# Kernel tuning notes

Hardware: AMD Instinct MI355X
Metric: run time of the kernel (lower is better)

Reference implementation:

```python
import jax, jax.numpy as jnp
import numpy as np
import itertools

D_FEAT = 8      # feature dim per point
N_NBR = 16     # kNN neighbors (self.N)
ORDERS = (2, 3)
BIG = 99999999.0


def _to_select(N, order):
    # rows: [0] + each (order-1)-combination of {1..N-1}, first N-1 rows
    rows = [[0] + list(c) for c in itertools.combinations(range(1, N), order - 1)][:N - 1]
    return np.asarray(rows, dtype=np.int32)  # (N-1, order)


def setup_inputs() -> dict:
    key = jax.random.key(0)
    ks = jax.random.split(key, 18)
    B, NP, DM, DO, NM, PNM = 4, 4096, 16, 8, 64, 64
    r = lambda k, s: jax.random.normal(k, s, dtype=jnp.float32)
    return {
        "x": r(ks[0], (B, NP * D_FEAT)),
        "z": r(ks[1], (B, PNM)),
        "Wm2": r(ks[2], (2, DM)) * 0.5, "bm2": r(ks[3], (DM,)) * 0.1,
        "Wm3": r(ks[4], (3, DM)) * 0.5, "bm3": r(ks[5], (DM,)) * 0.1,
        "Wv2": r(ks[6], (2, DM)) * 0.5, "bv2": r(ks[7], (DM,)) * 0.1,
        "Wv3": r(ks[8], (3, DM)) * 0.5, "bv3": r(ks[9], (DM,)) * 0.1,
        "Wmx": r(ks[10], (2 * DM, DO)) * 0.1, "bmx": r(ks[11], (DO,)) * 0.1,
        "Wvx": r(ks[12], (2 * DM, NM)) * 0.1, "bvx": r(ks[13], (NM,)) * 0.1,
        "Wmz": r(ks[14], (PNM, DO)) * 0.1, "bmz": r(ks[15], (DO,)) * 0.1,
        "Wvz": r(ks[16], (PNM, NM)) * 0.1, "bvz": r(ks[17], (NM,)) * 0.1,
    }


def _forward(x, z, Wm2, bm2, Wm3, bm3, Wv2, bv2, Wv3, bv3,
             Wmx, bmx, Wvx, bvx, Wmz, bmz, Wvz, bvz):
    B = x.shape[0]
    NP = x.shape[1] // D_FEAT
    N = N_NBR
    x3 = x.reshape(B, NP, D_FEAT)

    # pairwise euclidean distances via gram trick (avoids B*NP*NP*D intermediate)
    n2 = jnp.sum(x3 * x3, axis=-1)                                   # (B, NP)
    d2 = n2[:, :, None] + n2[:, None, :] - 2.0 * jnp.einsum('bid,bjd->bij', x3, x3)
    dist = jnp.sqrt(jnp.maximum(d2, 0.0))                            # (B, NP, NP)
    dist = jnp.where(dist == 0.0, BIG, dist)                         # mask exact-zero distances
    diag = jnp.arange(NP)
    dist = dist.at[:, diag, diag].set(BIG)                           # self-distance (exactly 0 in torch)

    # N smallest, sorted ascending
    _, idx = jax.lax.top_k(-dist, N)                                 # idx: (B, NP, N)

    def order_feats(Wf, bf, order):
        ts = jnp.asarray(_to_select(N, order))                       # (N-1, order)
        sel = idx[:, :, ts]                                          # (B, NP, N-1, o)
        g = jax.vmap(lambda xb, sb: xb[sb])(x3, sel)                 # (B, NP, N-1, o, D)
        # Linear(order -> d_Mfeat) applied per feature-dim o-tuple, relu, mean over feature dims
        y = jax.nn.relu(jnp.einsum('bnrod,ok->bnrdk', g, Wf) + bf)   # (B, NP, N-1, D, K)
        return y.mean(axis=3).reshape(B, NP * (N - 1), -1)           # (B, NP*(N-1), K)

    moments = jnp.concatenate([order_feats(Wm2, bm2, 2), order_feats(Wm3, bm3, 3)], axis=-1)
    v_moments = jnp.concatenate([order_feats(Wv2, bv2, 2), order_feats(Wv3, bv3, 3)], axis=-1)

    d_out = Wmx.shape[1]
    x_new = jax.nn.relu(moments @ Wmx + bmx + (z @ Wmz + bmz)[:, None, :])
    x_new = x_new.reshape(B, NP, N - 1, d_out).mean(axis=2).reshape(B, NP * d_out)

    z_new = jax.nn.relu(v_moments @ Wvx + bvx + (z @ Wvz + bvz)[:, None, :]).mean(axis=1)
    return x_new, z_new


def reference(x, z, Wm2, bm2, Wm3, bm3, Wv2, bv2, Wv3, bv3,
              Wmx, bmx, Wvx, bvx, Wmz, bmz, Wvz, bvz):
    return _forward(x, z, Wm2, bm2, Wm3, bm3, Wv2, bv2, Wv3, bv3,
                    Wmx, bmx, Wvx, bvx, Wmz, bmz, Wvz, bvz)
```

## Files before the change

kernel.cpp:

```cpp
#include <hip/hip_runtime.h>
#include <hip/hip_bf16.h>

#define BIGF 99999999.0f
#define NPP 4096
#define BB 4
#define NQ 4


__device__ __forceinline__ float rl(float v, int l) {
    return __int_as_float(__builtin_amdgcn_readlane(__float_as_int(v), l));
}

template <typename T>
__device__ __forceinline__ T bitonic_sort64(T v, int lane) {
    #pragma unroll
    for (int k = 2; k <= 64; k <<= 1) {
        #pragma unroll
        for (int j = k >> 1; j > 0; j >>= 1) {
            T p = __shfl_xor(v, j);
            bool up  = ((lane & k) == 0);
            bool low = ((lane & j) == 0);
            T mn = (v < p) ? v : p;
            T mx = (v < p) ? p : v;
            v = (up == low) ? mn : mx;
        }
    }
    return v;
}

__device__ __forceinline__ unsigned d2key(const float* qf, float n2i,
                                          const float4& a, const float4& c,
                                          float n2j, int j, int q) {
    float dot = 0.f;
    dot = fmaf(qf[0], a.x, dot); dot = fmaf(qf[1], a.y, dot);
    dot = fmaf(qf[2], a.z, dot); dot = fmaf(qf[3], a.w, dot);
    dot = fmaf(qf[4], c.x, dot); dot = fmaf(qf[5], c.y, dot);
    dot = fmaf(qf[6], c.z, dot); dot = fmaf(qf[7], c.w, dot);
    float d2 = fmaf(-2.0f, dot, n2i + n2j);
    return (d2 <= 0.0f || j == q) ? __float_as_uint(BIGF) : __float_as_uint(d2);
}


__global__ __launch_bounds__(256) void n2_kernel(const float* __restrict__ x,
                                                 float* __restrict__ n2tab,
                                                 float* __restrict__ zout) {
    int i = blockIdx.x * 256 + threadIdx.x;
    if (blockIdx.x == 0) zout[threadIdx.x] = 0.f;
    const float4* p = (const float4*)(x + (long)i * 8);
    float4 a = p[0], c = p[1];
    float s = 0.f;
    s = fmaf(a.x, a.x, s); s = fmaf(a.y, a.y, s);
    s = fmaf(a.z, a.z, s); s = fmaf(a.w, a.w, s);
    s = fmaf(c.x, c.x, s); s = fmaf(c.y, c.y, s);
    s = fmaf(c.z, c.z, s); s = fmaf(c.w, c.w, s);
    n2tab[i] = s;
}


__global__ void zz_kernel(const float* __restrict__ z,
                          const float* __restrict__ Wmz, const float* __restrict__ bmz,
                          const float* __restrict__ Wvz, const float* __restrict__ bvz,
                          float* __restrict__ zzm, float* __restrict__ zzv) {
    int b = blockIdx.x, l = threadIdx.x;
    float sv = 0.f;
    for (int p = 0; p < 64; ++p) sv = fmaf(z[b * 64 + p], Wvz[p * 64 + l], sv);
    zzv[b * 64 + l] = sv + bvz[l];
    if (l < 8) {
        float sm = 0.f;
        for (int p = 0; p < 64; ++p) sm = fmaf(z[b * 64 + p], Wmz[p * 8 + l], sm);
        zzm[b * 8 + l] = sm + bmz[l];
    }
}


__global__ __launch_bounds__(256) void knn_kernel(const float* __restrict__ x,
                                                  const float* __restrict__ n2tab,
                                                  int* __restrict__ idx_out) {
    __shared__ unsigned long long cand[4][NQ][64];

    int lane = threadIdx.x & 63;
    int wid  = threadIdx.x >> 6;
    int gw   = blockIdx.x * 4 + wid;
    int q0   = gw * NQ;
    int b    = q0 >> 12;
    int qloc = q0 & 4095;
    const float* xb = x + (long)b * NPP * 8;
    const float* nb = n2tab + b * NPP;

    float qf[NQ][8];
    float n2i[NQ];
    #pragma unroll
    for (int q = 0; q < NQ; ++q) {
        #pragma unroll
        for (int f = 0; f < 8; ++f) qf[q][f] = xb[(qloc + q) * 8 + f];
        n2i[q] = nb[qloc + q];
    }

    unsigned minb[NQ];
    #pragma unroll
    for (int q = 0; q < NQ; ++q) minb[q] = 0xFFFFFFFFu;

    #pragma unroll 4
    for (int t = 0; t < 64; ++t) {
        int j = t * 64 + lane;
        const float4* pj = (const float4*)(xb + j * 8);
        float4 a = pj[0], c = pj[1];
        float n2j = nb[j];
        #pragma unroll
        for (int q = 0; q < NQ; ++q) {
            unsigned kb = d2key(qf[q], n2i[q], a, c, n2j, j, qloc + q);
            minb[q] = (kb < minb[q]) ? kb : minb[q];
        }
    }

    unsigned T[NQ];
    #pragma unroll
    for (int q = 0; q < NQ; ++q) {
        unsigned v = bitonic_sort64(minb[q], lane);
        T[q] = (unsigned)__shfl((int)v, 15);
    }

    int cnt[NQ];
    #pragma unroll
    for (int q = 0; q < NQ; ++q) cnt[q] = 0;

    for (int t = 0; t < 64; ++t) {
        int j = t * 64 + lane;
        const float4* pj = (const float4*)(xb + j * 8);
        float4 a = pj[0], c = pj[1];
        float n2j = nb[j];
        #pragma unroll
        for (int q = 0; q < NQ; ++q) {
            unsigned kb = d2key(qf[q], n2i[q], a, c, n2j, j, qloc + q);
            bool pred = (kb <= T[q]);
            unsigned long long m = __ballot(pred);
            if (m) {
                int ofs = cnt[q] + __popcll(m & ((1ull << lane) - 1ull));
                if (pred && ofs < 64) {
                    cand[wid][q][ofs] = ((unsigned long long)kb << 32) | (unsigned)j;
                }
                cnt[q] += __popcll(m);
            }
        }
    }

    #pragma unroll 1
    for (int q = 0; q < NQ; ++q) {
        int c = cnt[q] < 64 ? cnt[q] : 64;
        unsigned long long key = (lane < c) ? cand[wid][q][lane] : ~0ull;
        key = bitonic_sort64(key, lane);
        if (lane < 16) {
            idx_out[(long)(q0 + q) * 16 + lane] = (int)(key & 0xFFFFFFFFull);
        }
    }
}


__global__ __launch_bounds__(256) void feat_kernel(
    const float* __restrict__ x, const int* __restrict__ idxw,
    const float* __restrict__ Wm2, const float* __restrict__ bm2,
    const float* __restrict__ Wm3, const float* __restrict__ bm3,
    const float* __restrict__ Wv2, const float* __restrict__ bv2,
    const float* __restrict__ Wv3, const float* __restrict__ bv3,
    const float* __restrict__ Wmx, const float* __restrict__ bmx,
    const float* __restrict__ Wvx, const float* __restrict__ bvx,
    const float* __restrict__ zzm, const float* __restrict__ zzv,
    float* __restrict__ xout, float* __restrict__ zout)
{
    int lane = threadIdx.x & 63;
    int wid  = threadIdx.x >> 6;
    int pn   = blockIdx.x * 4 + wid;
    int b    = pn >> 12;
    const float* xb = x + b * NPP * 8;

    __shared__ float xg_s[4][16][8];
    __shared__ float mm_s[4][15][36];
    __shared__ float wmx_s[32][8];
    __shared__ float bzm_s[8];
    __shared__ float zpart[4][64];

    if (threadIdx.x < 256) {
        wmx_s[threadIdx.x >> 3][threadIdx.x & 7] = Wmx[threadIdx.x];
    }
    if (threadIdx.x < 8) bzm_s[threadIdx.x] = bmx[threadIdx.x] + zzm[b * 8 + threadIdx.x];

    int k = lane & 15;
    float w20 = Wm2[k], w21 = Wm2[16 + k], bb2 = bm2[k];
    float w30 = Wm3[k], w31 = Wm3[16 + k], w32 = Wm3[32 + k], bb3 = bm3[k];
    float u20 = Wv2[k], u21 = Wv2[16 + k], cc2 = bv2[k];
    float u30 = Wv3[k], u31 = Wv3[16 + k], u32 = Wv3[32 + k], cc3 = bv3[k];
    float wvx[32];
    #pragma unroll
    for (int c = 0; c < 32; ++c) wvx[c] = Wvx[c * 64 + lane];
    float bz3 = bvx[lane] + zzv[b * 64 + lane];

    if (lane < 16) {
        int myid = idxw[(long)pn * 16 + lane];
        const float4* ps = (const float4*)(xb + (long)myid * 8);
        float4 a = ps[0], c4 = ps[1];
        *((float4*)&xg_s[wid][lane][0]) = a;
        *((float4*)&xg_s[wid][lane][4]) = c4;
    }
    __syncthreads();

    float g0[8];
    #pragma unroll
    for (int f = 0; f < 8; ++f) g0[f] = xg_s[wid][0][f];

    float am2[4], am3[4], av2[4], av3[4];
    #pragma unroll
    for (int p = 0; p < 4; ++p) {
        int rg = lane >> 4;
        int r  = p * 4 + rg;
        int rc = (r < 14) ? r : 14;
        int i2  = rc + 1;
        int i3a = (rc < 14) ? 1 : 2;
        int i3b = (rc < 14) ? rc + 2 : 3;
        const float* G1  = xg_s[wid][i2];
        const float* G3a = xg_s[wid][i3a];
        const float* G3b = xg_s[wid][i3b];
        float s2 = 0.f, s3 = 0.f, t2 = 0.f, t3 = 0.f;
        #pragma unroll
        for (int d = 0; d < 8; ++d) {
            float gz = g0[d], g1 = G1[d], ga = G3a[d], gb = G3b[d];
            float y2 = fmaf(gz, w20, fmaf(g1, w21, bb2));
            s2 += fmaxf(y2, 0.f);
            float y3 = fmaf(gz, w30, fmaf(ga, w31, fmaf(gb, w32, bb3)));
            s3 += fmaxf(y3, 0.f);
            float z2 = fmaf(gz, u20, fmaf(g1, u21, cc2));
            t2 += fmaxf(z2, 0.f);
            float z3 = fmaf(gz, u30, fmaf(ga, u31, fmaf(gb, u32, cc3)));
            t3 += fmaxf(z3, 0.f);
        }
        am2[p] = s2 * 0.125f; am3[p] = s3 * 0.125f;
        av2[p] = t2 * 0.125f; av3[p] = t3 * 0.125f;
        if (r < 15) {
            mm_s[wid][r][k]      = am2[p];
            mm_s[wid][r][16 + k] = am3[p];
        }
    }
    __syncthreads();

    float xa = 0.f;
    #pragma unroll
    for (int half = 0; half < 2; ++half) {
        int r   = (lane >> 3) + half * 8;
        int doo = lane & 7;
        float s = 0.f;
        if (r < 15) {
            s = bzm_s[doo];
            #pragma unroll
            for (int c = 0; c < 32; ++c)
                s = fmaf(mm_s[wid][r][c], wmx_s[c][doo], s);
            s = fmaxf(s, 0.f);
        }
        xa += s;
    }
    xa += __shfl_xor(xa, 8);
    xa += __shfl_xor(xa, 16);
    xa += __shfl_xor(xa, 32);
    float xv = xa * (1.0f / 15.0f);
    if (lane < 8) xout[(long)pn * 8 + lane] = xv;

    float za = 0.f;
    #pragma unroll
    for (int r = 0; r < 15; ++r) {
        float s = bz3;
        const int p  = r >> 2;
        const int sb = (r & 3) * 16;
        #pragma unroll
        for (int c = 0; c < 16; ++c)
            s = fmaf(rl(av2[p], sb + c), wvx[c], s);
        #pragma unroll
        for (int c = 0; c < 16; ++c)
            s = fmaf(rl(av3[p], sb + c), wvx[16 + c], s);
        za += fmaxf(s, 0.f);
    }
    za *= (1.0f / 61440.0f);

    zpart[wid][lane] = za;
    __syncthreads();
    if (wid == 0) {
        float ssum = zpart[0][lane] + zpart[1][lane] + zpart[2][lane] + zpart[3][lane];
        atomicAdd(&zout[b * 64 + lane], ssum);
    }
}


extern "C" void kernel_launch(void* const* d_in, const int* in_sizes, int n_in,
                              void* d_out, int out_size, void* d_ws, size_t ws_size,
                              hipStream_t stream) {
    const float* x   = (const float*)d_in[0];
    const float* z   = (const float*)d_in[1];
    const float* Wm2 = (const float*)d_in[2];
    const float* bm2 = (const float*)d_in[3];
    const float* Wm3 = (const float*)d_in[4];
    const float* bm3 = (const float*)d_in[5];
    const float* Wv2 = (const float*)d_in[6];
    const float* bv2 = (const float*)d_in[7];
    const float* Wv3 = (const float*)d_in[8];
    const float* bv3 = (const float*)d_in[9];
    const float* Wmx = (const float*)d_in[10];
    const float* bmx = (const float*)d_in[11];
    const float* Wvx = (const float*)d_in[12];
    const float* bvx = (const float*)d_in[13];
    const float* Wmz = (const float*)d_in[14];
    const float* bmz = (const float*)d_in[15];
    const float* Wvz = (const float*)d_in[16];
    const float* bvz = (const float*)d_in[17];

    float* out  = (float*)d_out;
    int*   idxw = (int*)d_ws;
    float* zzm  = (float*)((char*)d_ws + (size_t)BB * NPP * 16 * 4);
    float* zzv  = zzm + BB * 8;
    float* n2t  = zzv + BB * 64;
    float* xout = out;
    float* zout = out + BB * NPP * 8;

    n2_kernel<<<dim3(BB * NPP / 256), dim3(256), 0, stream>>>(x, n2t, zout);
    zz_kernel<<<dim3(BB), dim3(64), 0, stream>>>(z, Wmz, bmz, Wvz, bvz, zzm, zzv);
    knn_kernel<<<dim3(BB * NPP / (4 * NQ)), dim3(256), 0, stream>>>(x, n2t, idxw);
    feat_kernel<<<dim3(4096), dim3(256), 0, stream>>>(
        x, idxw, Wm2, bm2, Wm3, bm3, Wv2, bv2, Wv3, bv3,
        Wmx, bmx, Wvx, bvx, zzm, zzv, xout, zout);
}
```

Before: 266.7 us.

## Precompute kNN thresholds in separate kernel and merge larger candidate sets

Moves the threshold pass out of knn_kernel into a new thr_kernel. In it, each lane handles one query and takes minima over 16 strided stripes, and the maximum of those 16 minima serves as an upper bound for the 16th-nearest distance. knn_kernel then does only the ballot-compaction pass, with a larger candidate buffer (256 per query) and a chunked bitonic merge. The self-index check becomes cheaper and the zero-distance masking is dropped. The looser threshold lets more candidates through, which adds merge work and shared-memory use in exchange for removing one full distance pass per wavefront.

```diff
diff --git a/kernel.cpp b/kernel.cpp
--- a/kernel.cpp
+++ b/kernel.cpp
@@ -5,6 +5,7 @@
 #define NPP 4096
 #define BB 4
 #define NQ 4
+#define CAP 256
 
 
 __device__ __forceinline__ float rl(float v, int l) {
@@ -26,18 +27,6 @@
         }
     }
     return v;
-}
-
-__device__ __forceinline__ unsigned d2key(const float* qf, float n2i,
-                                          const float4& a, const float4& c,
-                                          float n2j, int j, int q) {
-    float dot = 0.f;
-    dot = fmaf(qf[0], a.x, dot); dot = fmaf(qf[1], a.y, dot);
-    dot = fmaf(qf[2], a.z, dot); dot = fmaf(qf[3], a.w, dot);
-    dot = fmaf(qf[4], c.x, dot); dot = fmaf(qf[5], c.y, dot);
-    dot = fmaf(qf[6], c.z, dot); dot = fmaf(qf[7], c.w, dot);
-    float d2 = fmaf(-2.0f, dot, n2i + n2j);
-    return (d2 <= 0.0f || j == q) ? __float_as_uint(BIGF) : __float_as_uint(d2);
 }
 
 
@@ -73,10 +62,65 @@
 }
 
 
+__global__ __launch_bounds__(512) void thr_kernel(const float* __restrict__ x,
+                                                  const float* __restrict__ n2tab,
+                                                  unsigned* __restrict__ Ttab) {
+    __shared__ unsigned mins_s[16][64];
+
+    int lane = threadIdx.x & 63;
+    int wid  = threadIdx.x >> 6;
+    int qg   = blockIdx.x * 64 + lane;
+    int b    = qg >> 12;
+    int qloc = qg & 4095;
+    const float* xb = x + (long)b * NPP * 8;
+    const float* nb = n2tab + b * NPP;
+
+    float qf[8];
+    #pragma unroll
+    for (int f = 0; f < 8; ++f) qf[f] = xb[(long)qloc * 8 + f];
+    float n2i = nb[qloc];
+    const unsigned BIGB = __float_as_uint(BIGF);
+
+    unsigned m0 = 0xFFFFFFFFu, m1 = 0xFFFFFFFFu;
+    int j0 = wid * 512;
+    #pragma unroll 4
+    for (int i = 0; i < 512; ++i) {
+        int j = j0 + i;
+        const float4* pj = (const float4*)(xb + (long)j * 8);
+        float4 a = pj[0], c = pj[1];
+        float n2j = nb[j];
+        float dot = 0.f;
+        dot = fmaf(qf[0], a.x, dot); dot = fmaf(qf[1], a.y, dot);
+        dot = fmaf(qf[2], a.z, dot); dot = fmaf(qf[3], a.w, dot);
+        dot = fmaf(qf[4], c.x, dot); dot = fmaf(qf[5], c.y, dot);
+        dot = fmaf(qf[6], c.z, dot); dot = fmaf(qf[7], c.w, dot);
+        float d2 = fmaf(-2.0f, dot, n2i + n2j);
+        unsigned kb = __float_as_uint(d2);
+        kb = (j == qloc) ? BIGB : kb;
+        if (i & 1) { m1 = (kb < m1) ? kb : m1; }
+        else       { m0 = (kb < m0) ? kb : m0; }
+    }
+    mins_s[wid * 2 + 0][lane] = m0;
+    mins_s[wid * 2 + 1][lane] = m1;
+    __syncthreads();
+
+    if (wid == 0) {
+        unsigned T = 0;
+        #pragma unroll
+        for (int i = 0; i < 16; ++i) {
+            unsigned v = mins_s[i][lane];
+            T = (v > T) ? v : T;
+        }
+        Ttab[blockIdx.x * 64 + lane] = T;
+    }
+}
+
+
 __global__ __launch_bounds__(256) void knn_kernel(const float* __restrict__ x,
                                                   const float* __restrict__ n2tab,
+                                                  const unsigned* __restrict__ Ttab,
                                                   int* __restrict__ idx_out) {
-    __shared__ unsigned long long cand[4][NQ][64];
+    __shared__ unsigned long long cand[4][NQ][CAP];
 
     int lane = threadIdx.x & 63;
     int wid  = threadIdx.x >> 6;
@@ -89,54 +133,45 @@
 
     float qf[NQ][8];
     float n2i[NQ];
+    unsigned Tq[NQ];
+    int cnt[NQ], selfT[NQ], selfL[NQ];
     #pragma unroll
     for (int q = 0; q < NQ; ++q) {
         #pragma unroll
         for (int f = 0; f < 8; ++f) qf[q][f] = xb[(qloc + q) * 8 + f];
-        n2i[q] = nb[qloc + q];
-    }
-
-    unsigned minb[NQ];
-    #pragma unroll
-    for (int q = 0; q < NQ; ++q) minb[q] = 0xFFFFFFFFu;
-
-    #pragma unroll 4
+        n2i[q]   = nb[qloc + q];
+        Tq[q]    = Ttab[q0 + q];
+        cnt[q]   = 0;
+        selfT[q] = (qloc + q) >> 6;
+        selfL[q] = (qloc + q) & 63;
+    }
+    const unsigned BIGB = __float_as_uint(BIGF);
+
     for (int t = 0; t < 64; ++t) {
         int j = t * 64 + lane;
-        const float4* pj = (const float4*)(xb + j * 8);
+        const float4* pj = (const float4*)(xb + (long)j * 8);
         float4 a = pj[0], c = pj[1];
         float n2j = nb[j];
         #pragma unroll
         for (int q = 0; q < NQ; ++q) {
-            unsigned kb = d2key(qf[q], n2i[q], a, c, n2j, j, qloc + q);
-            minb[q] = (kb < minb[q]) ? kb : minb[q];
-        }
-    }
-
-    unsigned T[NQ];
-    #pragma unroll
-    for (int q = 0; q < NQ; ++q) {
-        unsigned v = bitonic_sort64(minb[q], lane);
-        T[q] = (unsigned)__shfl((int)v, 15);
-    }
-
-    int cnt[NQ];
-    #pragma unroll
-    for (int q = 0; q < NQ; ++q) cnt[q] = 0;
-
-    for (int t = 0; t < 64; ++t) {
-        int j = t * 64 + lane;
-        const float4* pj = (const float4*)(xb + j * 8);
-        float4 a = pj[0], c = pj[1];
-        float n2j = nb[j];
-        #pragma unroll
-        for (int q = 0; q < NQ; ++q) {
-            unsigned kb = d2key(qf[q], n2i[q], a, c, n2j, j, qloc + q);
-            bool pred = (kb <= T[q]);
+            float dot = 0.f;
+            dot = fmaf(qf[q][0], a.x, dot); dot = fmaf(qf[q][1], a.y, dot);
+            dot = fmaf(qf[q][2], a.z, dot); dot = fmaf(qf[q][3], a.w, dot);
+            dot = fmaf(qf[q][4], c.x, dot); dot = fmaf(qf[q][5], c.y, dot);
+            dot = fmaf(qf[q][6], c.z, dot); dot = fmaf(qf[q][7], c.w, dot);
+            float d2 = fmaf(-2.0f, dot, n2i[q] + n2j);
+            unsigned kb = __float_as_uint(d2);
+            if (t == selfT[q]) {
+                kb = (lane == selfL[q]) ? BIGB : kb;
+            }
+            bool pred = (kb <= Tq[q]);
             unsigned long long m = __ballot(pred);
             if (m) {
-                int ofs = cnt[q] + __popcll(m & ((1ull << lane) - 1ull));
-                if (pred && ofs < 64) {
+                unsigned mlo = (unsigned)m, mhi = (unsigned)(m >> 32);
+                int below = __builtin_amdgcn_mbcnt_hi(mhi,
+                             __builtin_amdgcn_mbcnt_lo(mlo, 0));
+                int ofs = cnt[q] + below;
+                if (pred && ofs < CAP) {
                     cand[wid][q][ofs] = ((unsigned long long)kb << 32) | (unsigned)j;
                 }
                 cnt[q] += __popcll(m);
@@ -146,11 +181,21 @@
 
     #pragma unroll 1
     for (int q = 0; q < NQ; ++q) {
-        int c = cnt[q] < 64 ? cnt[q] : 64;
-        unsigned long long key = (lane < c) ? cand[wid][q][lane] : ~0ull;
-        key = bitonic_sort64(key, lane);
+        int n = cnt[q] > CAP ? CAP : cnt[q];
+        unsigned long long v = (lane < n) ? cand[wid][q][lane] : ~0ull;
+        unsigned long long R = bitonic_sort64(v, lane);
+        int nch = (n + 63) >> 6;
+        #pragma unroll 1
+        for (int cc = 1; cc < nch; ++cc) {
+            int base = cc << 6;
+            unsigned long long w2 = (base + lane < n) ? cand[wid][q][base + lane] : ~0ull;
+            w2 = bitonic_sort64(w2, lane);
+            unsigned long long vt = __shfl(w2, lane - 16);
+            unsigned long long comb = (lane < 16) ? R : ((lane < 32) ? vt : ~0ull);
+            R = bitonic_sort64(comb, lane);
+        }
         if (lane < 16) {
-            idx_out[(long)(q0 + q) * 16 + lane] = (int)(key & 0xFFFFFFFFull);
+            idx_out[(long)(q0 + q) * 16 + lane] = (int)(R & 0xFFFFFFFFull);
         }
     }
 }
@@ -314,12 +359,14 @@
     float* zzm  = (float*)((char*)d_ws + (size_t)BB * NPP * 16 * 4);
     float* zzv  = zzm + BB * 8;
     float* n2t  = zzv + BB * 64;
+    unsigned* Ttab = (unsigned*)(n2t + BB * NPP);
     float* xout = out;
     float* zout = out + BB * NPP * 8;
 
     n2_kernel<<<dim3(BB * NPP / 256), dim3(256), 0, stream>>>(x, n2t, zout);
     zz_kernel<<<dim3(BB), dim3(64), 0, stream>>>(z, Wmz, bmz, Wvz, bvz, zzm, zzv);
-    knn_kernel<<<dim3(BB * NPP / (4 * NQ)), dim3(256), 0, stream>>>(x, n2t, idxw);
+    thr_kernel<<<dim3(BB * NPP / 64), dim3(512), 0, stream>>>(x, n2t, Ttab);
+    knn_kernel<<<dim3(BB * NPP / (4 * NQ)), dim3(256), 0, stream>>>(x, n2t, Ttab, idxw);
     feat_kernel<<<dim3(4096), dim3(256), 0, stream>>>(
         x, idxw, Wm2, bm2, Wm3, bm3, Wv2, bv2, Wv3, bv3,
         Wmx, bmx, Wvx, bvx, zzm, zzv, xout, zout);
```

Measured after the change: 295.1 us. +10.6%, slower.
